# Kernel tuning notes

Hardware: AMD Instinct MI355X
Metric: run time of the kernel (lower is better)

Reference implementation:

```python
import jax, jax.numpy as jnp
import numpy as np


def setup_inputs() -> dict:
    key = jax.random.key(0)
    k1, k2 = jax.random.split(key)
    yhat = jax.random.normal(k1, (64, 128, 4096), dtype=jnp.float32)
    y = jax.random.normal(k2, (64, 128, 4096), dtype=jnp.float32)
    return {"yhat": yhat, "y": y}


def reference(yhat, y):
    # Original: sum over (batch, dim) of mean(|yhat[i,j] - y[i,j]|), divided by batch*dim.
    # All slices have identical size, so this equals the global L1 mean.
    return jnp.mean(jnp.abs(yhat - y))
```

## Files before the change

kernel.cpp:

```cpp
#include <hip/hip_runtime.h>

#define NBLOCKS 2048
#define NTHREADS 256

__global__ __launch_bounds__(NTHREADS) void l1_fused_kernel(
    const float4* __restrict__ a, const float4* __restrict__ b,
    const float* __restrict__ af, const float* __restrict__ bf,
    float* __restrict__ out, long n4, long n_total, float inv_n) {
    const long gid = (long)blockIdx.x * NTHREADS + threadIdx.x;
    const long stride = (long)NBLOCKS * NTHREADS;

    float acc0 = 0.f, acc1 = 0.f, acc2 = 0.f, acc3 = 0.f;
    long i = gid;
    for (; i + 3 * stride < n4; i += 4 * stride) {
        float4 x0 = a[i];
        float4 x1 = a[i + stride];
        float4 x2 = a[i + 2 * stride];
        float4 x3 = a[i + 3 * stride];
        float4 y0 = b[i];
        float4 y1 = b[i + stride];
        float4 y2 = b[i + 2 * stride];
        float4 y3 = b[i + 3 * stride];
        acc0 += fabsf(x0.x - y0.x) + fabsf(x0.y - y0.y) +
                fabsf(x0.z - y0.z) + fabsf(x0.w - y0.w);
        acc1 += fabsf(x1.x - y1.x) + fabsf(x1.y - y1.y) +
                fabsf(x1.z - y1.z) + fabsf(x1.w - y1.w);
        acc2 += fabsf(x2.x - y2.x) + fabsf(x2.y - y2.y) +
                fabsf(x2.z - y2.z) + fabsf(x2.w - y2.w);
        acc3 += fabsf(x3.x - y3.x) + fabsf(x3.y - y3.y) +
                fabsf(x3.z - y3.z) + fabsf(x3.w - y3.w);
    }
    for (; i < n4; i += stride) {
        float4 x = a[i];
        float4 y = b[i];
        acc0 += fabsf(x.x - y.x) + fabsf(x.y - y.y) +
                fabsf(x.z - y.z) + fabsf(x.w - y.w);
    }
    for (long e = n4 * 4 + gid; e < n_total; e += stride)
        acc0 += fabsf(af[e] - bf[e]);

    float acc = (acc0 + acc1) + (acc2 + acc3);

    #pragma unroll
    for (int off = 32; off > 0; off >>= 1)
        acc += __shfl_down(acc, off, 64);

    __shared__ float smem[NTHREADS / 64];
    int wave = threadIdx.x >> 6;
    int lane = threadIdx.x & 63;
    if (lane == 0) smem[wave] = acc;
    __syncthreads();
    if (threadIdx.x == 0) {
        float s = 0.f;
        #pragma unroll
        for (int w = 0; w < NTHREADS / 64; ++w) s += smem[w];
        atomicAdd(out, s * inv_n);
    }
}

extern "C" void kernel_launch(void* const* d_in, const int* in_sizes, int n_in,
                              void* d_out, int out_size, void* d_ws, size_t ws_size,
                              hipStream_t stream) {
    const float* yhat = (const float*)d_in[0];
    const float* y    = (const float*)d_in[1];
    float* out = (float*)d_out;

    long n = (long)in_sizes[0];
    long n4 = n / 4;
    float inv_n = 1.0f / (float)n;

    hipMemsetAsync(out, 0, sizeof(float), stream);
    l1_fused_kernel<<<NBLOCKS, NTHREADS, 0, stream>>>(
        (const float4*)yhat, (const float4*)y, yhat, y, out, n4, n, inv_n);
}
```

Measured before the change: 275.3 us.

## Switch to block-contiguous chunked loads with 8-way unrolled float4 reads

Changes the access pattern from a grid-strided interleave to per-block contiguous chunks of 256×8 float4s, issuing eight loads per input per iteration before accumulating. A minimum-occupancy hint of four blocks per CU is added to launch bounds. The aim is more bytes in flight per thread and better DRAM page locality for this bandwidth-bound reduction, at the cost of higher register pressure from sixteen float4 values held live.

Result: no change. 275.9 us (+0.2%).

```diff
diff --git a/kernel.cpp b/kernel.cpp
--- a/kernel.cpp
+++ b/kernel.cpp
@@ -2,55 +2,57 @@
 
 #define NBLOCKS 2048
 #define NTHREADS 256
+#define UNROLL 8
 
-__global__ __launch_bounds__(NTHREADS) void l1_fused_kernel(
+__global__ __launch_bounds__(NTHREADS, 4) void l1_fused_kernel(
     const float4* __restrict__ a, const float4* __restrict__ b,
     const float* __restrict__ af, const float* __restrict__ bf,
     float* __restrict__ out, long n4, long n_total, float inv_n) {
-    const long gid = (long)blockIdx.x * NTHREADS + threadIdx.x;
-    const long stride = (long)NBLOCKS * NTHREADS;
+    const int tid = threadIdx.x;
+    const long chunk = (long)NTHREADS * UNROLL;
+    const long nchunks = n4 / chunk;
 
-    float acc0 = 0.f, acc1 = 0.f, acc2 = 0.f, acc3 = 0.f;
-    long i = gid;
-    for (; i + 3 * stride < n4; i += 4 * stride) {
-        float4 x0 = a[i];
-        float4 x1 = a[i + stride];
-        float4 x2 = a[i + 2 * stride];
-        float4 x3 = a[i + 3 * stride];
-        float4 y0 = b[i];
-        float4 y1 = b[i + stride];
-        float4 y2 = b[i + 2 * stride];
-        float4 y3 = b[i + 3 * stride];
-        acc0 += fabsf(x0.x - y0.x) + fabsf(x0.y - y0.y) +
-                fabsf(x0.z - y0.z) + fabsf(x0.w - y0.w);
-        acc1 += fabsf(x1.x - y1.x) + fabsf(x1.y - y1.y) +
-                fabsf(x1.z - y1.z) + fabsf(x1.w - y1.w);
-        acc2 += fabsf(x2.x - y2.x) + fabsf(x2.y - y2.y) +
-                fabsf(x2.z - y2.z) + fabsf(x2.w - y2.w);
-        acc3 += fabsf(x3.x - y3.x) + fabsf(x3.y - y3.y) +
-                fabsf(x3.z - y3.z) + fabsf(x3.w - y3.w);
+    float acc[UNROLL];
+    #pragma unroll
+    for (int j = 0; j < UNROLL; ++j) acc[j] = 0.f;
+
+    for (long c = blockIdx.x; c < nchunks; c += NBLOCKS) {
+        const long base = c * chunk + tid;
+        float4 xs[UNROLL], ys[UNROLL];
+        #pragma unroll
+        for (int j = 0; j < UNROLL; ++j) xs[j] = a[base + j * NTHREADS];
+        #pragma unroll
+        for (int j = 0; j < UNROLL; ++j) ys[j] = b[base + j * NTHREADS];
+        #pragma unroll
+        for (int j = 0; j < UNROLL; ++j)
+            acc[j] += fabsf(xs[j].x - ys[j].x) + fabsf(xs[j].y - ys[j].y)
+                    + fabsf(xs[j].z - ys[j].z) + fabsf(xs[j].w - ys[j].w);
     }
-    for (; i < n4; i += stride) {
-        float4 x = a[i];
-        float4 y = b[i];
-        acc0 += fabsf(x.x - y.x) + fabsf(x.y - y.y) +
-                fabsf(x.z - y.z) + fabsf(x.w - y.w);
+
+    float racc = 0.f;
+    const long gid = (long)blockIdx.x * NTHREADS + tid;
+    const long tthreads = (long)NBLOCKS * NTHREADS;
+    for (long i = nchunks * chunk + gid; i < n4; i += tthreads) {
+        float4 x = a[i], y = b[i];
+        racc += fabsf(x.x - y.x) + fabsf(x.y - y.y)
+              + fabsf(x.z - y.z) + fabsf(x.w - y.w);
     }
-    for (long e = n4 * 4 + gid; e < n_total; e += stride)
-        acc0 += fabsf(af[e] - bf[e]);
+    for (long e = n4 * 4 + gid; e < n_total; e += tthreads)
+        racc += fabsf(af[e] - bf[e]);
 
-    float acc = (acc0 + acc1) + (acc2 + acc3);
+    float acc_total = ((acc[0] + acc[1]) + (acc[2] + acc[3]))
+                    + ((acc[4] + acc[5]) + (acc[6] + acc[7])) + racc;
 
     #pragma unroll
     for (int off = 32; off > 0; off >>= 1)
-        acc += __shfl_down(acc, off, 64);
+        acc_total += __shfl_down(acc_total, off, 64);
 
     __shared__ float smem[NTHREADS / 64];
-    int wave = threadIdx.x >> 6;
-    int lane = threadIdx.x & 63;
-    if (lane == 0) smem[wave] = acc;
+    int wave = tid >> 6;
+    int lane = tid & 63;
+    if (lane == 0) smem[wave] = acc_total;
     __syncthreads();
-    if (threadIdx.x == 0) {
+    if (tid == 0) {
         float s = 0.f;
         #pragma unroll
         for (int w = 0; w < NTHREADS / 64; ++w) s += smem[w];
```
